# Kernel optimization log

Measured on AMD Instinct MI355X. Metric: run time of the kernel, lower is better.

## Reference

```python
import jax, jax.numpy as jnp
import numpy as np

S, C1, C2, N = 4096, 2048, 2048, 1024


def setup_inputs() -> dict:
    key = jax.random.key(0)
    k1, k2, k3, k4 = jax.random.split(key, 4)
    # child log-likelihoods (samples, child_nodes); modest scale so exp() stays finite,
    # matching the (numerically naive) torch forward which exps without max-subtraction.
    ll1 = jax.random.normal(k1, (S, C1), dtype=jnp.float32)
    ll2 = jax.random.normal(k2, (S, C2), dtype=jnp.float32)
    # log edge weights, one tensor per child layer: (nodes, child_nodes)
    w1 = jax.random.normal(k3, (N, C1), dtype=jnp.float32)
    w2 = jax.random.normal(k4, (N, C2), dtype=jnp.float32)
    return {"ll1": ll1, "ll2": ll2, "w1": w1, "w2": w2}


def reference(ll1, ll2, w1, w2):
    # Per child layer: sum_c exp(ll[s,c] + w[n,c]) == exp(ll) @ exp(w).T  -> (S, N)
    # (same math as unsqueeze/repeat/exp/sum in the torch code, without the (S,C,N) blowup)
    result = jnp.exp(ll1) @ jnp.exp(w1).T + jnp.exp(ll2) @ jnp.exp(w2).T  # (S, N)
    # per-node log normalization constant over concatenated weights
    log_z = jax.nn.logsumexp(jnp.concatenate([w1, w2], axis=1), axis=1)  # (N,)
    return jnp.log(result) - log_z[None, :]
```

## Files before the change

kernel.cpp:

```cpp
#include <hip/hip_runtime.h>

#define S_DIM 4096
#define C_DIM 2048
#define N_DIM 1024
#define K_DIM 4096

#define BM 128
#define BN 128
#define BK 32
#define NT (K_DIM / BK)
#define TILE_BYTES 16384
#define NBUF 8

typedef __attribute__((ext_vector_type(8))) short bf16x8;
typedef __attribute__((ext_vector_type(4))) float f32x4;

__device__ static inline unsigned short f2bf(float f) {
    unsigned int u = __float_as_uint(f);
    u += 0x7FFFu + ((u >> 16) & 1u);
    return (unsigned short)(u >> 16);
}

__global__ void exp_ll_kernel(const float* __restrict__ ll1,
                              const float* __restrict__ ll2,
                              unsigned short* __restrict__ A) {
    const int total4 = S_DIM * C_DIM / 4;
    int stride = gridDim.x * blockDim.x;
    for (int i = blockIdx.x * blockDim.x + threadIdx.x; i < total4; i += stride) {
        int e = i << 2;
        int r = e >> 11;
        int c = e & 2047;
        size_t dst = ((size_t)r << 12) + c;
        float4 v = *reinterpret_cast<const float4*>(ll1 + e);
        ushort4 o;
        o.x = f2bf(__expf(v.x)); o.y = f2bf(__expf(v.y));
        o.z = f2bf(__expf(v.z)); o.w = f2bf(__expf(v.w));
        *reinterpret_cast<ushort4*>(A + dst) = o;
        float4 u = *reinterpret_cast<const float4*>(ll2 + e);
        ushort4 p;
        p.x = f2bf(__expf(u.x)); p.y = f2bf(__expf(u.y));
        p.z = f2bf(__expf(u.z)); p.w = f2bf(__expf(u.w));
        *reinterpret_cast<ushort4*>(A + dst + C_DIM) = p;
    }
}

__global__ void w_kernel(const float* __restrict__ w1,
                         const float* __restrict__ w2,
                         unsigned short* __restrict__ B,
                         float* __restrict__ lz) {
    const int n = blockIdx.x;
    const int tid = threadIdx.x;
    const int lane = tid & 63, wv = tid >> 6;
    const float* r1 = w1 + ((size_t)n << 11);
    const float* r2 = w2 + ((size_t)n << 11);
    float4 v0 = *reinterpret_cast<const float4*>(r1 + tid * 8);
    float4 v1 = *reinterpret_cast<const float4*>(r1 + tid * 8 + 4);
    float4 u0 = *reinterpret_cast<const float4*>(r2 + tid * 8);
    float4 u1 = *reinterpret_cast<const float4*>(r2 + tid * 8 + 4);

    float mx = fmaxf(fmaxf(fmaxf(v0.x, v0.y), fmaxf(v0.z, v0.w)),
                     fmaxf(fmaxf(v1.x, v1.y), fmaxf(v1.z, v1.w)));
    mx = fmaxf(mx, fmaxf(fmaxf(fmaxf(u0.x, u0.y), fmaxf(u0.z, u0.w)),
                          fmaxf(fmaxf(u1.x, u1.y), fmaxf(u1.z, u1.w))));
    #pragma unroll
    for (int off = 32; off > 0; off >>= 1) mx = fmaxf(mx, __shfl_xor(mx, off));
    __shared__ float red[4];
    if (lane == 0) red[wv] = mx;
    __syncthreads();
    mx = fmaxf(fmaxf(red[0], red[1]), fmaxf(red[2], red[3]));

    float s = __expf(v0.x - mx) + __expf(v0.y - mx) + __expf(v0.z - mx) + __expf(v0.w - mx)
            + __expf(v1.x - mx) + __expf(v1.y - mx) + __expf(v1.z - mx) + __expf(v1.w - mx)
            + __expf(u0.x - mx) + __expf(u0.y - mx) + __expf(u0.z - mx) + __expf(u0.w - mx)
            + __expf(u1.x - mx) + __expf(u1.y - mx) + __expf(u1.z - mx) + __expf(u1.w - mx);
    #pragma unroll
    for (int off = 32; off > 0; off >>= 1) s += __shfl_xor(s, off);
    __shared__ float red2[4];
    if (lane == 0) red2[wv] = s;
    __syncthreads();
    if (tid == 0)
        lz[n] = mx + __logf(red2[0] + red2[1] + red2[2] + red2[3]);

    unsigned short* brow = B + ((size_t)n << 12);
    ushort4 o;
    o.x = f2bf(__expf(v0.x)); o.y = f2bf(__expf(v0.y));
    o.z = f2bf(__expf(v0.z)); o.w = f2bf(__expf(v0.w));
    *reinterpret_cast<ushort4*>(brow + tid * 8) = o;
    o.x = f2bf(__expf(v1.x)); o.y = f2bf(__expf(v1.y));
    o.z = f2bf(__expf(v1.z)); o.w = f2bf(__expf(v1.w));
    *reinterpret_cast<ushort4*>(brow + tid * 8 + 4) = o;
    o.x = f2bf(__expf(u0.x)); o.y = f2bf(__expf(u0.y));
    o.z = f2bf(__expf(u0.z)); o.w = f2bf(__expf(u0.w));
    *reinterpret_cast<ushort4*>(brow + C_DIM + tid * 8) = o;
    o.x = f2bf(__expf(u1.x)); o.y = f2bf(__expf(u1.y));
    o.z = f2bf(__expf(u1.z)); o.w = f2bf(__expf(u1.w));
    *reinterpret_cast<ushort4*>(brow + C_DIM + tid * 8 + 4) = o;
}

typedef const unsigned int __attribute__((address_space(1)))* gas_ptr;
typedef unsigned int __attribute__((address_space(3)))* las_ptr;

__global__ __launch_bounds__(256, 1) void gemm_log_kernel(
        const unsigned short* __restrict__ A,
        const unsigned short* __restrict__ B,
        const float* __restrict__ lz,
        float* __restrict__ out) {
    __shared__ __align__(16) char lds[NBUF * TILE_BYTES];
    const int tid  = threadIdx.x;
    const int l    = tid & 63;
    const int w    = tid >> 6;
    const int bn = blockIdx.x & 7;
    const int bm = blockIdx.x >> 3;
    const int wr = w >> 1, wc = w & 1;
    const int lcol = l & 15, lk = l >> 4;

    const int kg = (l & 3) ^ ((l >> 3) & 3);
    const unsigned short* src[4];
    int dst[4];
    #pragma unroll
    for (int i = 0; i < 4; ++i) {
        const int ri  = w * 4 + i;
        const int row = ri * 16 + (l >> 2);
        src[i] = (ri < 8)
            ? A + (size_t)(bm * BM + row) * K_DIM + kg * 8
            : B + (size_t)(bn * BN + row - 128) * K_DIM + kg * 8;
        dst[i] = row * 64 + (l & 3) * 16;
    }

    const int swz = (lk ^ ((lcol >> 1) & 3)) << 4;
    int aoff[4], boff[4];
    #pragma unroll
    for (int m = 0; m < 4; ++m) aoff[m] = (wr * 64 + m * 16 + lcol) * 64 + swz;
    #pragma unroll
    for (int n = 0; n < 4; ++n) boff[n] = 8192 + (wc * 64 + n * 16 + lcol) * 64 + swz;

    f32x4 acc[4][4] = {};
    bf16x8 a0[4], b0[4], a1[4], b1[4];

#define GLOAD(p, o) __builtin_amdgcn_global_load_lds((gas_ptr)(const void*)(p), \
        (las_ptr)(void*)(lds + (o)), 16, 0, 0)
#define STAGE(T, BUFI) { const int _ko = (T) * BK; const int _bo = (BUFI) * TILE_BYTES; \
        GLOAD(src[0] + _ko, _bo + dst[0]); GLOAD(src[1] + _ko, _bo + dst[1]);           \
        GLOAD(src[2] + _ko, _bo + dst[2]); GLOAD(src[3] + _ko, _bo + dst[3]); }
#define READF(RBUF, AR, BR) { const char* _rb = lds + (RBUF) * TILE_BYTES;              \
        _Pragma("unroll") for (int m = 0; m < 4; ++m)                                   \
            AR[m] = *reinterpret_cast<const bf16x8*>(_rb + aoff[m]);                    \
        _Pragma("unroll") for (int n = 0; n < 4; ++n)                                   \
            BR[n] = *reinterpret_cast<const bf16x8*>(_rb + boff[n]); }
#define MFMAS(AMM, BMM)                                                                 \
        _Pragma("unroll") for (int m = 0; m < 4; ++m)                                   \
            _Pragma("unroll") for (int n = 0; n < 4; ++n)                               \
                acc[m][n] = __builtin_amdgcn_mfma_f32_16x16x32_bf16(AMM[m], BMM[n],     \
                                                                    acc[m][n], 0, 0, 0);
#define BODY(T, SB, RB, WAITN, DOSTAGE, AR, BR, AMM, BMM) {                             \
        asm volatile("s_waitcnt vmcnt(" #WAITN ")" ::: "memory");                       \
        __builtin_amdgcn_s_barrier();                                                   \
        if (DOSTAGE) STAGE((T) + 8, SB);                                                \
        READF(RB, AR, BR);                                                              \
        MFMAS(AMM, BMM); }

    STAGE(0, 0); STAGE(1, 1); STAGE(2, 2); STAGE(3, 3);
    STAGE(4, 4); STAGE(5, 5); STAGE(6, 6); STAGE(7, 7);
    asm volatile("s_waitcnt vmcnt(28)" ::: "memory");
    __builtin_amdgcn_s_barrier();
    READF(0, a0, b0);

    for (int t8 = 0; t8 < NT - 8; t8 += 8) {
        BODY(t8 + 0, 0, 1, 24, 1, a1, b1, a0, b0);
        BODY(t8 + 1, 1, 2, 24, 1, a0, b0, a1, b1);
        BODY(t8 + 2, 2, 3, 24, 1, a1, b1, a0, b0);
        BODY(t8 + 3, 3, 4, 24, 1, a0, b0, a1, b1);
        BODY(t8 + 4, 4, 5, 24, 1, a1, b1, a0, b0);
        BODY(t8 + 5, 5, 6, 24, 1, a0, b0, a1, b1);
        BODY(t8 + 6, 6, 7, 24, 1, a1, b1, a0, b0);
        BODY(t8 + 7, 7, 0, 24, 1, a0, b0, a1, b1);
    }
    BODY(120, 0, 1, 24, 0, a1, b1, a0, b0);
    BODY(121, 1, 2, 20, 0, a0, b0, a1, b1);
    BODY(122, 2, 3, 16, 0, a1, b1, a0, b0);
    BODY(123, 3, 4, 12, 0, a0, b0, a1, b1);
    BODY(124, 4, 5,  8, 0, a1, b1, a0, b0);
    BODY(125, 5, 6,  4, 0, a0, b0, a1, b1);
    BODY(126, 6, 7,  0, 0, a1, b1, a0, b0);
    MFMAS(a1, b1);
#undef BODY
#undef MFMAS
#undef READF
#undef STAGE
#undef GLOAD

    const int col_base = bn * BN + wc * 64;
    float lzv[4];
    #pragma unroll
    for (int n = 0; n < 4; ++n) lzv[n] = lz[col_base + n * 16 + lcol];
    #pragma unroll
    for (int m = 0; m < 4; ++m) {
        const int row0 = bm * BM + wr * 64 + m * 16 + lk * 4;
        #pragma unroll
        for (int n = 0; n < 4; ++n) {
            const int col = col_base + n * 16 + lcol;
            #pragma unroll
            for (int j = 0; j < 4; ++j)
                out[(size_t)(row0 + j) * N_DIM + col] = __logf(acc[m][n][j]) - lzv[n];
        }
    }
}

__global__ void naive_kernel(const float* __restrict__ ll1, const float* __restrict__ ll2,
                             const float* __restrict__ w1, const float* __restrict__ w2,
                             float* __restrict__ out) {
    int idx = blockIdx.x * blockDim.x + threadIdx.x;
    if (idx >= S_DIM * N_DIM) return;
    int s = idx >> 10, n = idx & (N_DIM - 1);
    const float* a1 = ll1 + (size_t)s * C_DIM;
    const float* a2 = ll2 + (size_t)s * C_DIM;
    const float* b1 = w1 + (size_t)n * C_DIM;
    const float* b2 = w2 + (size_t)n * C_DIM;
    float mx = -3.0e38f;
    for (int c = 0; c < C_DIM; ++c) mx = fmaxf(mx, b1[c]);
    for (int c = 0; c < C_DIM; ++c) mx = fmaxf(mx, b2[c]);
    float zs = 0.f, acc = 0.f;
    for (int c = 0; c < C_DIM; ++c) { zs += __expf(b1[c] - mx); acc += __expf(a1[c] + b1[c]); }
    for (int c = 0; c < C_DIM; ++c) { zs += __expf(b2[c] - mx); acc += __expf(a2[c] + b2[c]); }
    out[idx] = __logf(acc) - (mx + __logf(zs));
}

extern "C" void kernel_launch(void* const* d_in, const int* in_sizes, int n_in,
                              void* d_out, int out_size, void* d_ws, size_t ws_size,
                              hipStream_t stream) {
    const float* ll1 = (const float*)d_in[0];
    const float* ll2 = (const float*)d_in[1];
    const float* w1  = (const float*)d_in[2];
    const float* w2  = (const float*)d_in[3];
    float* out = (float*)d_out;

    const size_t a_elems = (size_t)S_DIM * K_DIM;
    const size_t b_elems = (size_t)N_DIM * K_DIM;
    const size_t need = (a_elems + b_elems) * sizeof(unsigned short) + N_DIM * sizeof(float);
    if (ws_size < need) {
        naive_kernel<<<(S_DIM * N_DIM + 255) / 256, 256, 0, stream>>>(ll1, ll2, w1, w2, out);
        return;
    }
    unsigned short* Aws = (unsigned short*)d_ws;
    unsigned short* Bws = Aws + a_elems;
    float* lzws = (float*)(Bws + b_elems);

    exp_ll_kernel<<<2048, 256, 0, stream>>>(ll1, ll2, Aws);
    w_kernel<<<N_DIM, 256, 0, stream>>>(w1, w2, Bws, lzws);
    gemm_log_kernel<<<(S_DIM / BM) * (N_DIM / BN), 256, 0, stream>>>(Aws, Bws, lzws, out);
}
```

Baseline: 71.05 us.

## Warp-specialize GEMM into producer load waves and consumer MFMA waves

Doubles the block to 512 threads: four waves now only issue the global-to-LDS async loads into the 8-deep ring buffer, and four waves only read LDS and run MFMAs. The two groups stay in step through matching per-stage barriers, and the vmcnt waits move to the producer side only. MFMA sections are wrapped in s_setprio so compute waves get issue priority over the load waves. The aim is to take load issue and wait instructions off the compute waves' critical path. The cost is extra waves and barrier participants, and the 128KB LDS footprint still allows only one block per CU despite the new launch bounds.

```diff
diff --git a/kernel.cpp b/kernel.cpp
--- a/kernel.cpp
+++ b/kernel.cpp
@@ -100,7 +100,7 @@
 typedef const unsigned int __attribute__((address_space(1)))* gas_ptr;
 typedef unsigned int __attribute__((address_space(3)))* las_ptr;
 
-__global__ __launch_bounds__(256, 1) void gemm_log_kernel(
+__global__ __launch_bounds__(512, 2) void gemm_log_kernel(
         const unsigned short* __restrict__ A,
         const unsigned short* __restrict__ B,
         const float* __restrict__ lz,
@@ -111,99 +111,122 @@
     const int w    = tid >> 6;
     const int bn = blockIdx.x & 7;
     const int bm = blockIdx.x >> 3;
-    const int wr = w >> 1, wc = w & 1;
-    const int lcol = l & 15, lk = l >> 4;
-
-    const int kg = (l & 3) ^ ((l >> 3) & 3);
-    const unsigned short* src[4];
-    int dst[4];
-    #pragma unroll
-    for (int i = 0; i < 4; ++i) {
-        const int ri  = w * 4 + i;
-        const int row = ri * 16 + (l >> 2);
-        src[i] = (ri < 8)
-            ? A + (size_t)(bm * BM + row) * K_DIM + kg * 8
-            : B + (size_t)(bn * BN + row - 128) * K_DIM + kg * 8;
-        dst[i] = row * 64 + (l & 3) * 16;
-    }
-
-    const int swz = (lk ^ ((lcol >> 1) & 3)) << 4;
-    int aoff[4], boff[4];
-    #pragma unroll
-    for (int m = 0; m < 4; ++m) aoff[m] = (wr * 64 + m * 16 + lcol) * 64 + swz;
-    #pragma unroll
-    for (int n = 0; n < 4; ++n) boff[n] = 8192 + (wc * 64 + n * 16 + lcol) * 64 + swz;
-
-    f32x4 acc[4][4] = {};
-    bf16x8 a0[4], b0[4], a1[4], b1[4];
-
-#define GLOAD(p, o) __builtin_amdgcn_global_load_lds((gas_ptr)(const void*)(p), \
-        (las_ptr)(void*)(lds + (o)), 16, 0, 0)
+
+#define GLOAD(p_, o_) __builtin_amdgcn_global_load_lds((gas_ptr)(const void*)(p_), \
+        (las_ptr)(void*)(lds + (o_)), 16, 0, 0)
+
+    if (w >= 4) {
+        const int pw = w - 4;
+        const int kg = (l & 3) ^ ((l >> 3) & 3);
+        const unsigned short* src[4];
+        int dst[4];
+        #pragma unroll
+        for (int i = 0; i < 4; ++i) {
+            const int ri  = pw * 4 + i;
+            const int row = ri * 16 + (l >> 2);
+            src[i] = (ri < 8)
+                ? A + (size_t)(bm * BM + row) * K_DIM + kg * 8
+                : B + (size_t)(bn * BN + row - 128) * K_DIM + kg * 8;
+            dst[i] = row * 64 + (l & 3) * 16;
+        }
 #define STAGE(T, BUFI) { const int _ko = (T) * BK; const int _bo = (BUFI) * TILE_BYTES; \
         GLOAD(src[0] + _ko, _bo + dst[0]); GLOAD(src[1] + _ko, _bo + dst[1]);           \
         GLOAD(src[2] + _ko, _bo + dst[2]); GLOAD(src[3] + _ko, _bo + dst[3]); }
+#define PBODY(T, BUFI, WAITN) {                                                         \
+        asm volatile("s_waitcnt vmcnt(" #WAITN ")" ::: "memory");                       \
+        __builtin_amdgcn_s_barrier();                                                   \
+        STAGE((T) + 8, BUFI); }
+
+        STAGE(0, 0); STAGE(1, 1); STAGE(2, 2); STAGE(3, 3);
+        STAGE(4, 4); STAGE(5, 5); STAGE(6, 6); STAGE(7, 7);
+        asm volatile("s_waitcnt vmcnt(28)" ::: "memory");
+        __builtin_amdgcn_s_barrier();
+        for (int t8 = 0; t8 < NT - 8; t8 += 8) {
+            PBODY(t8 + 0, 0, 24); PBODY(t8 + 1, 1, 24);
+            PBODY(t8 + 2, 2, 24); PBODY(t8 + 3, 3, 24);
+            PBODY(t8 + 4, 4, 24); PBODY(t8 + 5, 5, 24);
+            PBODY(t8 + 6, 6, 24); PBODY(t8 + 7, 7, 24);
+        }
+        asm volatile("s_waitcnt vmcnt(24)" ::: "memory"); __builtin_amdgcn_s_barrier();
+        asm volatile("s_waitcnt vmcnt(20)" ::: "memory"); __builtin_amdgcn_s_barrier();
+        asm volatile("s_waitcnt vmcnt(16)" ::: "memory"); __builtin_amdgcn_s_barrier();
+        asm volatile("s_waitcnt vmcnt(12)" ::: "memory"); __builtin_amdgcn_s_barrier();
+        asm volatile("s_waitcnt vmcnt(8)"  ::: "memory"); __builtin_amdgcn_s_barrier();
+        asm volatile("s_waitcnt vmcnt(4)"  ::: "memory"); __builtin_amdgcn_s_barrier();
+        asm volatile("s_waitcnt vmcnt(0)"  ::: "memory"); __builtin_amdgcn_s_barrier();
+#undef PBODY
+#undef STAGE
+    } else {
+        const int wr = w >> 1, wc = w & 1;
+        const int lcol = l & 15, lk = l >> 4;
+        const int swz = (lk ^ ((lcol >> 1) & 3)) << 4;
+        int aoff[4], boff[4];
+        #pragma unroll
+        for (int m = 0; m < 4; ++m) aoff[m] = (wr * 64 + m * 16 + lcol) * 64 + swz;
+        #pragma unroll
+        for (int n = 0; n < 4; ++n) boff[n] = 8192 + (wc * 64 + n * 16 + lcol) * 64 + swz;
+
+        f32x4 acc[4][4] = {};
+        bf16x8 a0[4], b0[4], a1[4], b1[4];
+
 #define READF(RBUF, AR, BR) { const char* _rb = lds + (RBUF) * TILE_BYTES;              \
         _Pragma("unroll") for (int m = 0; m < 4; ++m)                                   \
             AR[m] = *reinterpret_cast<const bf16x8*>(_rb + aoff[m]);                    \
         _Pragma("unroll") for (int n = 0; n < 4; ++n)                                   \
             BR[n] = *reinterpret_cast<const bf16x8*>(_rb + boff[n]); }
-#define MFMAS(AMM, BMM)                                                                 \
+#define MFMAS(AMM, BMM) {                                                               \
+        __builtin_amdgcn_s_setprio(1);                                                  \
         _Pragma("unroll") for (int m = 0; m < 4; ++m)                                   \
             _Pragma("unroll") for (int n = 0; n < 4; ++n)                               \
                 acc[m][n] = __builtin_amdgcn_mfma_f32_16x16x32_bf16(AMM[m], BMM[n],     \
-                                                                    acc[m][n], 0, 0, 0);
-#define BODY(T, SB, RB, WAITN, DOSTAGE, AR, BR, AMM, BMM) {                             \
-        asm volatile("s_waitcnt vmcnt(" #WAITN ")" ::: "memory");                       \
+                                                                    acc[m][n], 0, 0, 0);\
+        __builtin_amdgcn_s_setprio(0); }
+#define CBODY(T, RB, AR, BR, AMM, BMM) {                                                \
         __builtin_amdgcn_s_barrier();                                                   \
-        if (DOSTAGE) STAGE((T) + 8, SB);                                                \
         READF(RB, AR, BR);                                                              \
         MFMAS(AMM, BMM); }
 
-    STAGE(0, 0); STAGE(1, 1); STAGE(2, 2); STAGE(3, 3);
-    STAGE(4, 4); STAGE(5, 5); STAGE(6, 6); STAGE(7, 7);
-    asm volatile("s_waitcnt vmcnt(28)" ::: "memory");
-    __builtin_amdgcn_s_barrier();
-    READF(0, a0, b0);
-
-    for (int t8 = 0; t8 < NT - 8; t8 += 8) {
-        BODY(t8 + 0, 0, 1, 24, 1, a1, b1, a0, b0);
-        BODY(t8 + 1, 1, 2, 24, 1, a0, b0, a1, b1);
-        BODY(t8 + 2, 2, 3, 24, 1, a1, b1, a0, b0);
-        BODY(t8 + 3, 3, 4, 24, 1, a0, b0, a1, b1);
-        BODY(t8 + 4, 4, 5, 24, 1, a1, b1, a0, b0);
-        BODY(t8 + 5, 5, 6, 24, 1, a0, b0, a1, b1);
-        BODY(t8 + 6, 6, 7, 24, 1, a1, b1, a0, b0);
-        BODY(t8 + 7, 7, 0, 24, 1, a0, b0, a1, b1);
-    }
-    BODY(120, 0, 1, 24, 0, a1, b1, a0, b0);
-    BODY(121, 1, 2, 20, 0, a0, b0, a1, b1);
-    BODY(122, 2, 3, 16, 0, a1, b1, a0, b0);
-    BODY(123, 3, 4, 12, 0, a0, b0, a1, b1);
-    BODY(124, 4, 5,  8, 0, a1, b1, a0, b0);
-    BODY(125, 5, 6,  4, 0, a0, b0, a1, b1);
-    BODY(126, 6, 7,  0, 0, a1, b1, a0, b0);
-    MFMAS(a1, b1);
-#undef BODY
+        __builtin_amdgcn_s_barrier();
+        READF(0, a0, b0);
+        for (int t8 = 0; t8 < NT - 8; t8 += 8) {
+            CBODY(t8 + 0, 1, a1, b1, a0, b0);
+            CBODY(t8 + 1, 2, a0, b0, a1, b1);
+            CBODY(t8 + 2, 3, a1, b1, a0, b0);
+            CBODY(t8 + 3, 4, a0, b0, a1, b1);
+            CBODY(t8 + 4, 5, a1, b1, a0, b0);
+            CBODY(t8 + 5, 6, a0, b0, a1, b1);
+            CBODY(t8 + 6, 7, a1, b1, a0, b0);
+            CBODY(t8 + 7, 0, a0, b0, a1, b1);
+        }
+        CBODY(120, 1, a1, b1, a0, b0);
+        CBODY(121, 2, a0, b0, a1, b1);
+        CBODY(122, 3, a1, b1, a0, b0);
+        CBODY(123, 4, a0, b0, a1, b1);
+        CBODY(124, 5, a1, b1, a0, b0);
+        CBODY(125, 6, a0, b0, a1, b1);
+        CBODY(126, 7, a1, b1, a0, b0);
+        MFMAS(a1, b1);
+#undef CBODY
 #undef MFMAS
 #undef READF
-#undef STAGE
+
+        const int col_base = bn * BN + wc * 64;
+        float lzv[4];
+        #pragma unroll
+        for (int n = 0; n < 4; ++n) lzv[n] = lz[col_base + n * 16 + lcol];
+        #pragma unroll
+        for (int m = 0; m < 4; ++m) {
+            const int row0 = bm * BM + wr * 64 + m * 16 + lk * 4;
+            #pragma unroll
+            for (int n = 0; n < 4; ++n) {
+                const int col = col_base + n * 16 + lcol;
+                #pragma unroll
+                for (int j = 0; j < 4; ++j)
+                    out[(size_t)(row0 + j) * N_DIM + col] = __logf(acc[m][n][j]) - lzv[n];
+            }
+        }
+    }
 #undef GLOAD
-
-    const int col_base = bn * BN + wc * 64;
-    float lzv[4];
-    #pragma unroll
-    for (int n = 0; n < 4; ++n) lzv[n] = lz[col_base + n * 16 + lcol];
-    #pragma unroll
-    for (int m = 0; m < 4; ++m) {
-        const int row0 = bm * BM + wr * 64 + m * 16 + lk * 4;
-        #pragma unroll
-        for (int n = 0; n < 4; ++n) {
-            const int col = col_base + n * 16 + lcol;
-            #pragma unroll
-            for (int j = 0; j < 4; ++j)
-                out[(size_t)(row0 + j) * N_DIM + col] = __logf(acc[m][n][j]) - lzv[n];
-        }
-    }
 }
 
 __global__ void naive_kernel(const float* __restrict__ ll1, const float* __restrict__ ll2,
@@ -247,5 +270,5 @@
 
     exp_ll_kernel<<<2048, 256, 0, stream>>>(ll1, ll2, Aws);
     w_kernel<<<N_DIM, 256, 0, stream>>>(w1, w2, Bws, lzws);
-    gemm_log_kernel<<<(S_DIM / BM) * (N_DIM / BN), 256, 0, stream>>>(Aws, Bws, lzws, out);
-}
+    gemm_log_kernel<<<(S_DIM / BM) * (N_DIM / BN), 512, 0, stream>>>(Aws, Bws, lzws, out);
+}
```

Measured after the change: 70.77 us. No clear change (-0.4%).

## Add split-K 256x256 GEMM with bf16 partials and separate log-reduce kernel

Applied to the files above, without the earlier changes.

Adds a path that tiles the GEMM into 256x256 blocks with 8 waves, splits K into four slices, and launches 256 workgroups. Each workgroup writes bf16 partial sums to workspace, and a separate kernel adds the four partials and applies log and the normalizer. The larger tile raises data reuse per LDS load while the K split keeps all CUs busy. In exchange it adds about 32MB of partial-sum traffic, an extra launch, and bf16 rounding of partials, which lowers accuracy. The old 128x128 kernel remains as a fallback when workspace is small.

```diff
diff --git a/kernel.cpp b/kernel.cpp
--- a/kernel.cpp
+++ b/kernel.cpp
@@ -5,20 +5,32 @@
 #define N_DIM 1024
 #define K_DIM 4096
 
-#define BM 128
-#define BN 128
+#define BM2 256
+#define BN2 256
+#define KS 4
+#define KSL (K_DIM / KS)
 #define BK 32
-#define NT (K_DIM / BK)
-#define TILE_BYTES 16384
-#define NBUF 8
+#define NT2 (KSL / BK)
+#define TILE2 32768
+#define NBUF2 4
+
+#define BM1 128
+#define BN1 128
+#define NT1 (K_DIM / BK)
+#define TILE1 16384
+#define NBUF1 8
 
 typedef __attribute__((ext_vector_type(8))) short bf16x8;
+typedef __attribute__((ext_vector_type(8))) unsigned short u16x8;
 typedef __attribute__((ext_vector_type(4))) float f32x4;
 
 __device__ static inline unsigned short f2bf(float f) {
     unsigned int u = __float_as_uint(f);
     u += 0x7FFFu + ((u >> 16) & 1u);
     return (unsigned short)(u >> 16);
+}
+__device__ static inline float bf2f(unsigned short h) {
+    return __uint_as_float((unsigned int)h << 16);
 }
 
 __global__ void exp_ll_kernel(const float* __restrict__ ll1,
@@ -100,12 +112,133 @@
 typedef const unsigned int __attribute__((address_space(1)))* gas_ptr;
 typedef unsigned int __attribute__((address_space(3)))* las_ptr;
 
-__global__ __launch_bounds__(256, 1) void gemm_log_kernel(
+__global__ __launch_bounds__(512, 1) void gemm_split_kernel(
+        const unsigned short* __restrict__ A,
+        const unsigned short* __restrict__ B,
+        unsigned short* __restrict__ P) {
+    __shared__ __align__(16) char lds[NBUF2 * TILE2];
+    const int tid  = threadIdx.x;
+    const int l    = tid & 63;
+    const int w    = tid >> 6;
+    const int wg   = blockIdx.x;
+    const int x7   = wg & 7;
+    const int bm   = (wg >> 3) & 15;
+    const int c    = x7 + ((wg >> 7) << 3);
+    const int ks   = c >> 2;
+    const int bn   = c & 3;
+    const int wr = w >> 1, wc = w & 1;
+    const int lcol = l & 15, lk = l >> 4;
+
+    const int kg = (l & 3) ^ ((l >> 3) & 3);
+    const unsigned short* src[4];
+    int dst[4];
+    #pragma unroll
+    for (int i = 0; i < 4; ++i) {
+        const int ri  = w + i * 8;
+        const int row = ri * 16 + (l >> 2);
+        src[i] = (i < 2)
+            ? A + (size_t)(bm * BM2 + row) * K_DIM + ks * KSL + kg * 8
+            : B + (size_t)(bn * BN2 + row - 256) * K_DIM + ks * KSL + kg * 8;
+        dst[i] = row * 64 + (l & 3) * 16;
+    }
+
+    const int swz = (lk ^ ((lcol >> 1) & 3)) << 4;
+    int aoff[4], boff[8];
+    #pragma unroll
+    for (int m = 0; m < 4; ++m) aoff[m] = (wr * 64 + m * 16 + lcol) * 64 + swz;
+    #pragma unroll
+    for (int n = 0; n < 8; ++n) boff[n] = 16384 + (wc * 128 + n * 16 + lcol) * 64 + swz;
+
+    f32x4 acc[4][8] = {};
+    bf16x8 a[4], b[8];
+
+#define GLOAD(p_, o_) __builtin_amdgcn_global_load_lds((gas_ptr)(const void*)(p_), \
+        (las_ptr)(void*)(lds + (o_)), 16, 0, 0)
+#define STAGE2(T, BUFI) { const int _ko = (T) * BK; const int _bo = (BUFI) * TILE2; \
+        GLOAD(src[0] + _ko, _bo + dst[0]); GLOAD(src[1] + _ko, _bo + dst[1]);       \
+        GLOAD(src[2] + _ko, _bo + dst[2]); GLOAD(src[3] + _ko, _bo + dst[3]); }
+#define READF2(RBUF) { const char* _rb = lds + (RBUF) * TILE2;                      \
+        _Pragma("unroll") for (int m = 0; m < 4; ++m)                               \
+            a[m] = *reinterpret_cast<const bf16x8*>(_rb + aoff[m]);                 \
+        _Pragma("unroll") for (int n = 0; n < 8; ++n)                               \
+            b[n] = *reinterpret_cast<const bf16x8*>(_rb + boff[n]); }
+#define MFMAS2() {                                                                  \
+        __builtin_amdgcn_s_setprio(1);                                              \
+        _Pragma("unroll") for (int m = 0; m < 4; ++m)                               \
+            _Pragma("unroll") for (int n = 0; n < 8; ++n)                           \
+                acc[m][n] = __builtin_amdgcn_mfma_f32_16x16x32_bf16(a[m], b[n],     \
+                                                                    acc[m][n], 0, 0, 0); \
+        __builtin_amdgcn_s_setprio(0); }
+#define BODY2(RBUF, TS, SBUF, WAITN, DOSTAGE) {                                     \
+        asm volatile("s_waitcnt vmcnt(" #WAITN ")" ::: "memory");                   \
+        __builtin_amdgcn_s_barrier();                                               \
+        if (DOSTAGE) STAGE2(TS, SBUF);                                              \
+        READF2(RBUF);                                                               \
+        MFMAS2(); }
+
+    STAGE2(0, 0); STAGE2(1, 1); STAGE2(2, 2);
+    for (int t4 = 0; t4 < NT2 - 4; t4 += 4) {
+        BODY2(0, t4 + 3, 3, 8, 1);
+        BODY2(1, t4 + 4, 0, 8, 1);
+        BODY2(2, t4 + 5, 1, 8, 1);
+        BODY2(3, t4 + 6, 2, 8, 1);
+    }
+    BODY2(0, 31, 3, 8, 1);
+    BODY2(1, 0, 0, 8, 0);
+    BODY2(2, 0, 0, 4, 0);
+    BODY2(3, 0, 0, 0, 0);
+#undef BODY2
+#undef MFMAS2
+#undef READF2
+#undef STAGE2
+
+    unsigned short* Pk = P + (size_t)ks * ((size_t)S_DIM * N_DIM);
+    const int col_base = bn * BN2 + wc * 128;
+    #pragma unroll
+    for (int m = 0; m < 4; ++m) {
+        const int row0 = bm * BM2 + wr * 64 + m * 16 + lk * 4;
+        #pragma unroll
+        for (int n = 0; n < 8; ++n) {
+            const int col = col_base + n * 16 + lcol;
+            #pragma unroll
+            for (int j = 0; j < 4; ++j)
+                Pk[(size_t)(row0 + j) * N_DIM + col] = f2bf(acc[m][n][j]);
+        }
+    }
+#undef GLOAD
+}
+
+__global__ void reduce_kernel(const unsigned short* __restrict__ P,
+                              const float* __restrict__ lz,
+                              float* __restrict__ out) {
+    const size_t SN = (size_t)S_DIM * N_DIM;
+    int i = blockIdx.x * blockDim.x + threadIdx.x;
+    size_t e = (size_t)i * 8;
+    int n = (int)(e & (N_DIM - 1));
+    u16x8 p0 = *reinterpret_cast<const u16x8*>(P + e);
+    u16x8 p1 = *reinterpret_cast<const u16x8*>(P + SN + e);
+    u16x8 p2 = *reinterpret_cast<const u16x8*>(P + 2 * SN + e);
+    u16x8 p3 = *reinterpret_cast<const u16x8*>(P + 3 * SN + e);
+    float4 lz0 = *reinterpret_cast<const float4*>(lz + n);
+    float4 lz1 = *reinterpret_cast<const float4*>(lz + n + 4);
+    float lzv[8] = {lz0.x, lz0.y, lz0.z, lz0.w, lz1.x, lz1.y, lz1.z, lz1.w};
+    float o[8];
+    #pragma unroll
+    for (int j = 0; j < 8; ++j) {
+        float s = bf2f((unsigned short)p0[j]) + bf2f((unsigned short)p1[j])
+                + bf2f((unsigned short)p2[j]) + bf2f((unsigned short)p3[j]);
+        o[j] = __logf(s) - lzv[j];
+    }
+    *reinterpret_cast<float4*>(out + e)     = make_float4(o[0], o[1], o[2], o[3]);
+    *reinterpret_cast<float4*>(out + e + 4) = make_float4(o[4], o[5], o[6], o[7]);
+}
+
+__global__ __launch_bounds__(256, 1) void gemm_log_kernel128(
         const unsigned short* __restrict__ A,
         const unsigned short* __restrict__ B,
         const float* __restrict__ lz,
         float* __restrict__ out) {
-    __shared__ __align__(16) char lds[NBUF * TILE_BYTES];
+    __shared__ __align__(16) char lds[NBUF1 * TILE1];
     const int tid  = threadIdx.x;
     const int l    = tid & 63;
     const int w    = tid >> 6;
@@ -122,11 +255,10 @@
         const int ri  = w * 4 + i;
         const int row = ri * 16 + (l >> 2);
         src[i] = (ri < 8)
-            ? A + (size_t)(bm * BM + row) * K_DIM + kg * 8
-            : B + (size_t)(bn * BN + row - 128) * K_DIM + kg * 8;
+            ? A + (size_t)(bm * BM1 + row) * K_DIM + kg * 8
+            : B + (size_t)(bn * BN1 + row - 128) * K_DIM + kg * 8;
         dst[i] = row * 64 + (l & 3) * 16;
     }
-
     const int swz = (lk ^ ((lcol >> 1) & 3)) << 4;
     int aoff[4], boff[4];
     #pragma unroll
@@ -137,26 +269,26 @@
     f32x4 acc[4][4] = {};
     bf16x8 a0[4], b0[4], a1[4], b1[4];
 
-#define GLOAD(p, o) __builtin_amdgcn_global_load_lds((gas_ptr)(const void*)(p), \
-        (las_ptr)(void*)(lds + (o)), 16, 0, 0)
-#define STAGE(T, BUFI) { const int _ko = (T) * BK; const int _bo = (BUFI) * TILE_BYTES; \
-        GLOAD(src[0] + _ko, _bo + dst[0]); GLOAD(src[1] + _ko, _bo + dst[1]);           \
+#define GLOAD(p_, o_) __builtin_amdgcn_global_load_lds((gas_ptr)(const void*)(p_), \
+        (las_ptr)(void*)(lds + (o_)), 16, 0, 0)
+#define STAGE(T, BUFI) { const int _ko = (T) * BK; const int _bo = (BUFI) * TILE1; \
+        GLOAD(src[0] + _ko, _bo + dst[0]); GLOAD(src[1] + _ko, _bo + dst[1]);      \
         GLOAD(src[2] + _ko, _bo + dst[2]); GLOAD(src[3] + _ko, _bo + dst[3]); }
-#define READF(RBUF, AR, BR) { const char* _rb = lds + (RBUF) * TILE_BYTES;              \
-        _Pragma("unroll") for (int m = 0; m < 4; ++m)                                   \
-            AR[m] = *reinterpret_cast<const bf16x8*>(_rb + aoff[m]);                    \
-        _Pragma("unroll") for (int n = 0; n < 4; ++n)                                   \
+#define READF(RBUF, AR, BR) { const char* _rb = lds + (RBUF) * TILE1;              \
+        _Pragma("unroll") for (int m = 0; m < 4; ++m)                              \
+            AR[m] = *reinterpret_cast<const bf16x8*>(_rb + aoff[m]);               \
+        _Pragma("unroll") for (int n = 0; n < 4; ++n)                              \
             BR[n] = *reinterpret_cast<const bf16x8*>(_rb + boff[n]); }
-#define MFMAS(AMM, BMM)                                                                 \
-        _Pragma("unroll") for (int m = 0; m < 4; ++m)                                   \
-            _Pragma("unroll") for (int n = 0; n < 4; ++n)                               \
-                acc[m][n] = __builtin_amdgcn_mfma_f32_16x16x32_bf16(AMM[m], BMM[n],     \
+#define MFMAS(AMM, BMM)                                                            \
+        _Pragma("unroll") for (int m = 0; m < 4; ++m)                              \
+            _Pragma("unroll") for (int n = 0; n < 4; ++n)                          \
+                acc[m][n] = __builtin_amdgcn_mfma_f32_16x16x32_bf16(AMM[m], BMM[n],\
                                                                     acc[m][n], 0, 0, 0);
-#define BODY(T, SB, RB, WAITN, DOSTAGE, AR, BR, AMM, BMM) {                             \
-        asm volatile("s_waitcnt vmcnt(" #WAITN ")" ::: "memory");                       \
-        __builtin_amdgcn_s_barrier();                                                   \
-        if (DOSTAGE) STAGE((T) + 8, SB);                                                \
-        READF(RB, AR, BR);                                                              \
+#define BODY(T, SB, RB, WAITN, DOSTAGE, AR, BR, AMM, BMM) {                        \
+        asm volatile("s_waitcnt vmcnt(" #WAITN ")" ::: "memory");                  \
+        __builtin_amdgcn_s_barrier();                                              \
+        if (DOSTAGE) STAGE((T) + 8, SB);                                           \
+        READF(RB, AR, BR);                                                         \
         MFMAS(AMM, BMM); }
 
     STAGE(0, 0); STAGE(1, 1); STAGE(2, 2); STAGE(3, 3);
@@ -164,8 +296,7 @@
     asm volatile("s_waitcnt vmcnt(28)" ::: "memory");
     __builtin_amdgcn_s_barrier();
     READF(0, a0, b0);
-
-    for (int t8 = 0; t8 < NT - 8; t8 += 8) {
+    for (int t8 = 0; t8 < NT1 - 8; t8 += 8) {
         BODY(t8 + 0, 0, 1, 24, 1, a1, b1, a0, b0);
         BODY(t8 + 1, 1, 2, 24, 1, a0, b0, a1, b1);
         BODY(t8 + 2, 2, 3, 24, 1, a1, b1, a0, b0);
@@ -189,13 +320,13 @@
 #undef STAGE
 #undef GLOAD
 
-    const int col_base = bn * BN + wc * 64;
+    const int col_base = bn * BN1 + wc * 64;
     float lzv[4];
     #pragma unroll
     for (int n = 0; n < 4; ++n) lzv[n] = lz[col_base + n * 16 + lcol];
     #pragma unroll
     for (int m = 0; m < 4; ++m) {
-        const int row0 = bm * BM + wr * 64 + m * 16 + lk * 4;
+        const int row0 = bm * BM1 + wr * 64 + m * 16 + lk * 4;
         #pragma unroll
         for (int n = 0; n < 4; ++n) {
             const int col = col_base + n * 16 + lcol;
@@ -236,8 +367,10 @@
 
     const size_t a_elems = (size_t)S_DIM * K_DIM;
     const size_t b_elems = (size_t)N_DIM * K_DIM;
-    const size_t need = (a_elems + b_elems) * sizeof(unsigned short) + N_DIM * sizeof(float);
-    if (ws_size < need) {
+    const size_t sn      = (size_t)S_DIM * N_DIM;
+    const size_t need1 = (a_elems + b_elems) * sizeof(unsigned short) + N_DIM * sizeof(float);
+    const size_t need2 = need1 + KS * sn * sizeof(unsigned short);
+    if (ws_size < need1) {
         naive_kernel<<<(S_DIM * N_DIM + 255) / 256, 256, 0, stream>>>(ll1, ll2, w1, w2, out);
         return;
     }
@@ -247,5 +380,12 @@
 
     exp_ll_kernel<<<2048, 256, 0, stream>>>(ll1, ll2, Aws);
     w_kernel<<<N_DIM, 256, 0, stream>>>(w1, w2, Bws, lzws);
-    gemm_log_kernel<<<(S_DIM / BM) * (N_DIM / BN), 256, 0, stream>>>(Aws, Bws, lzws, out);
-}
+
+    if (ws_size >= need2) {
+        unsigned short* Pws = (unsigned short*)(lzws + N_DIM);
+        gemm_split_kernel<<<(S_DIM / BM2) * (N_DIM / BN2) * KS, 512, 0, stream>>>(Aws, Bws, Pws);
+        reduce_kernel<<<(int)(sn / 8 / 256), 256, 0, stream>>>(Pws, lzws, out);
+    } else {
+        gemm_log_kernel128<<<(S_DIM / BM1) * (N_DIM / BN1), 256, 0, stream>>>(Aws, Bws, lzws, out);
+    }
+}
```

Result: slower. 73.67 us (+3.7%).
